# Kernel optimization log

Hardware: AMD Instinct MI355X
Metric: run time of the kernel (lower is better)

The kernel has to match this reference:

```python
import jax, jax.numpy as jnp
import numpy as np
import math

D = 1024
H = 16
HD = D // H
P = 64  # bias_proj_dim
B, N, M = 4, 1024, 2048
EPS_LN = 1e-5
EPS_NORM = 1e-12


def _ln(x, g, b):
    mu = jnp.mean(x, axis=-1, keepdims=True)
    var = jnp.var(x, axis=-1, keepdims=True)
    return (x - mu) * jax.lax.rsqrt(var + EPS_LN) * g + b


def _l2norm_dim1(x):
    # torch F.normalize(x, p=2) default dim=1 -> normalize over the sequence axis
    n = jnp.sqrt(jnp.sum(x * x, axis=1, keepdims=True))
    return x / jnp.maximum(n, EPS_NORM)


def setup_inputs() -> dict:
    key = jax.random.key(0)
    ks = jax.random.split(key, 16)
    s = 1.0 / math.sqrt(D)
    inp = {
        'dataset_features': jax.random.normal(ks[0], (B, N, D), jnp.float32),
        'visual_features': jax.random.normal(ks[1], (B, M, D), jnp.float32),
        # linear weights stored as (in, out): y = x @ W + b
        'wq_w': jax.random.normal(ks[2], (D, D), jnp.float32) * s,
        'wq_b': jnp.zeros((D,), jnp.float32),
        'wk_w': jax.random.normal(ks[3], (D, D), jnp.float32) * s,
        'wk_b': jnp.zeros((D,), jnp.float32),
        'wv_w': jax.random.normal(ks[4], (D, D), jnp.float32) * s,
        'wv_b': jnp.zeros((D,), jnp.float32),
        'wo_w': jax.random.normal(ks[5], (D, D), jnp.float32) * s,
        'wo_b': jnp.zeros((D,), jnp.float32),
        'gq_w': jax.random.normal(ks[6], (D, P), jnp.float32) * s,
        'gq_b': jnp.zeros((P,), jnp.float32),
        'gk_w': jax.random.normal(ks[7], (D, P), jnp.float32) * s,
        'gk_b': jnp.zeros((P,), jnp.float32),
        'pos_scale': jnp.asarray(2.0, jnp.float32),
        'neg_scale': jnp.asarray(50.0, jnp.float32),
        'attn_logit_scale': jnp.asarray(math.log(10.0), jnp.float32),
        'ln_q_g': jnp.ones((D,), jnp.float32),
        'ln_q_b': jnp.zeros((D,), jnp.float32),
        'ln_kv_g': jnp.ones((D,), jnp.float32),
        'ln_kv_b': jnp.zeros((D,), jnp.float32),
        'ln_out_g': jnp.ones((D,), jnp.float32),
        'ln_out_b': jnp.zeros((D,), jnp.float32),
        'ff1_w': jax.random.normal(ks[8], (D, 2 * D), jnp.float32) * s,
        'ff1_b': jnp.zeros((2 * D,), jnp.float32),
        'ff2_w': jax.random.normal(ks[9], (2 * D, D), jnp.float32) * (1.0 / math.sqrt(2 * D)),
        'ff2_b': jnp.zeros((D,), jnp.float32),
    }
    return inp


def reference(dataset_features, visual_features, wq_w, wq_b, wk_w, wk_b, wv_w, wv_b,
              wo_w, wo_b, gq_w, gq_b, gk_w, gk_b, pos_scale, neg_scale,
              attn_logit_scale, ln_q_g, ln_q_b, ln_kv_g, ln_kv_b, ln_out_g, ln_out_b,
              ff1_w, ff1_b, ff2_w, ff2_b):
    residual = dataset_features
    q_in = _ln(dataset_features, ln_q_g, ln_q_b)   # [B,N,D]
    kv_in = _ln(visual_features, ln_kv_g, ln_kv_b)  # [B,M,D]

    geo_q = _l2norm_dim1(q_in @ gq_w + gq_b)   # [B,N,P], normalized over N
    geo_k = _l2norm_dim1(kv_in @ gk_w + gk_b)  # [B,M,P], normalized over M
    bias_raw = jnp.einsum('bnp,bmp->bnm', geo_q, geo_k)  # [B,N,M]
    full_bias = jax.nn.relu(bias_raw) * pos_scale - jax.nn.relu(-bias_raw) * neg_scale

    q = (q_in @ wq_w + wq_b).reshape(B, N, H, HD).transpose(0, 2, 1, 3)   # [B,H,N,hd]
    k = (kv_in @ wk_w + wk_b).reshape(B, M, H, HD).transpose(0, 2, 1, 3)  # [B,H,M,hd]
    v = (kv_in @ wv_w + wv_b).reshape(B, M, H, HD).transpose(0, 2, 1, 3)

    logits = jnp.einsum('bhnd,bhmd->bhnm', q, k) / math.sqrt(HD)
    logits = logits * jnp.exp(attn_logit_scale)
    scores = logits + full_bias[:, None, :, :]
    attn = jax.nn.softmax(scores, axis=-1)
    out = jnp.einsum('bhnm,bhmd->bhnd', attn, v).transpose(0, 2, 1, 3).reshape(B, N, D)
    out = out @ wo_w + wo_b
    out = residual + out

    residual = out
    h = _ln(out, ln_out_g, ln_out_b)
    ff = jax.nn.gelu(h @ ff1_w + ff1_b, approximate=False) @ ff2_w + ff2_b
    return residual + ff
```

## Files before the change

kernel.cpp:

```cpp
#include <hip/hip_runtime.h>


typedef __bf16 bf16x8 __attribute__((ext_vector_type(8)));
typedef __bf16 bf16x4 __attribute__((ext_vector_type(4)));
typedef float  f32x4  __attribute__((ext_vector_type(4)));

__device__ inline f32x4 mfma16(bf16x8 a, bf16x8 b, f32x4 c) {
  return __builtin_amdgcn_mfma_f32_16x16x32_bf16(a, b, c, 0, 0, 0);
}

__device__ inline void glds16(const void* g, void* l) {
  __builtin_amdgcn_global_load_lds(
      (const __attribute__((address_space(1))) void*)g,
      (__attribute__((address_space(3))) void*)l, 16, 0, 0);
}

__device__ inline int swz(int row, int col) {
  return row * 64 + ((((col >> 3) ^ (row & 7)) << 3) | (col & 7));
}

#define DB 1024
#define DH 16
#define DHD 64
#define DP 64
#define NB 4
#define NN 1024
#define NM 2048

__global__ __launch_bounds__(256) void k_transpose_all(
    const float* __restrict__ w0, const float* __restrict__ w1,
    const float* __restrict__ w2, const float* __restrict__ w3,
    const float* __restrict__ f1, const float* __restrict__ f2,
    const float* __restrict__ g0, const float* __restrict__ g1,
    __bf16* __restrict__ o0, __bf16* __restrict__ o1,
    __bf16* __restrict__ o2, __bf16* __restrict__ o3,
    __bf16* __restrict__ of1, __bf16* __restrict__ of2,
    __bf16* __restrict__ og0, __bf16* __restrict__ og1) {
  __shared__ float tile[32][33];
  int id = blockIdx.x;
  const float* in;
  __bf16* out;
  int K, O, x, y;
  if (id < 4096) {
    int mi = id >> 10, r = id & 1023;
    in = mi == 0 ? w0 : mi == 1 ? w1 : mi == 2 ? w2 : w3;
    out = mi == 0 ? o0 : mi == 1 ? o1 : mi == 2 ? o2 : o3;
    K = 1024; O = 1024; x = r & 31; y = r >> 5;
  } else if (id < 6144) {
    int r = id - 4096; in = f1; out = of1; K = 1024; O = 2048; x = r & 63; y = r >> 6;
  } else if (id < 8192) {
    int r = id - 6144; in = f2; out = of2; K = 2048; O = 1024; x = r & 31; y = r >> 5;
  } else if (id < 8256) {
    int r = id - 8192; in = g0; out = og0; K = 1024; O = 64; x = r & 1; y = r >> 1;
  } else {
    int r = id - 8256; in = g1; out = og1; K = 1024; O = 64; x = r & 1; y = r >> 1;
  }
  int k0 = y * 32, o0c = x * 32;
  int tx = threadIdx.x & 31, ty = threadIdx.x >> 5;
#pragma unroll
  for (int r = ty; r < 32; r += 8)
    tile[r][tx] = in[(size_t)(k0 + r) * O + (o0c + tx)];
  __syncthreads();
#pragma unroll
  for (int r = ty; r < 32; r += 8)
    out[(size_t)(o0c + r) * K + (k0 + tx)] = (__bf16)tile[tx][r];
}

__device__ inline void ln_body(const float* __restrict__ x,
                               const float* __restrict__ g,
                               const float* __restrict__ bb,
                               __bf16* __restrict__ y, size_t row) {
  int t = threadIdx.x;
  float4 v = ((const float4*)(x + row * 1024))[t];
  float s = v.x + v.y + v.z + v.w;
  float ss = v.x * v.x + v.y * v.y + v.z * v.z + v.w * v.w;
#pragma unroll
  for (int o = 32; o; o >>= 1) {
    s += __shfl_down(s, o, 64);
    ss += __shfl_down(ss, o, 64);
  }
  __shared__ float r1[4], r2[4];
  if ((t & 63) == 0) { r1[t >> 6] = s; r2[t >> 6] = ss; }
  __syncthreads();
  s = r1[0] + r1[1] + r1[2] + r1[3];
  ss = r2[0] + r2[1] + r2[2] + r2[3];
  float mu = s * (1.f / 1024.f);
  float rstd = rsqrtf(ss * (1.f / 1024.f) - mu * mu + 1e-5f);
  float4 gv = ((const float4*)g)[t];
  float4 bv = ((const float4*)bb)[t];
  __bf16* yr = y + row * 1024 + t * 4;
  yr[0] = (__bf16)((v.x - mu) * rstd * gv.x + bv.x);
  yr[1] = (__bf16)((v.y - mu) * rstd * gv.y + bv.y);
  yr[2] = (__bf16)((v.z - mu) * rstd * gv.z + bv.z);
  yr[3] = (__bf16)((v.w - mu) * rstd * gv.w + bv.w);
}

__global__ __launch_bounds__(256) void k_layernorm(
    const float* __restrict__ x, const float* __restrict__ g,
    const float* __restrict__ bb, __bf16* __restrict__ y) {
  ln_body(x, g, bb, y, blockIdx.x);
}

__global__ __launch_bounds__(256) void k_layernorm2(
    const float* __restrict__ x1, const float* __restrict__ g1,
    const float* __restrict__ b1, __bf16* __restrict__ y1,
    const float* __restrict__ x2, const float* __restrict__ g2,
    const float* __restrict__ b2, __bf16* __restrict__ y2) {
  int row = blockIdx.x;
  if (row < 4096) ln_body(x1, g1, b1, y1, row);
  else ln_body(x2, g2, b2, y2, row - 4096);
}

__global__ __launch_bounds__(256) void k_geo(
    const __bf16* __restrict__ qin, const __bf16* __restrict__ kvin,
    const __bf16* __restrict__ gqw, const __bf16* __restrict__ gkw,
    const float* __restrict__ gqb, const float* __restrict__ gkb,
    __bf16* __restrict__ geoq, __bf16* __restrict__ geok) {
  const int blk = blockIdx.x;
  const bool isq = blk < 128;
  const __bf16* A = isq ? qin : kvin;
  const __bf16* Bt = isq ? gqw : gkw;
  const float* bias = isq ? gqb : gkb;
  __bf16* C = isq ? geoq : geok;
  const int row0 = (isq ? blk : blk - 128) * 32;
  __shared__ __align__(16) __bf16 As[32][72], Bs[64][72];
  const int t = threadIdx.x, lane = t & 63, w = t >> 6;
  const int quad = lane >> 4, l15 = lane & 15;
  const int wr = w >> 1, wc = w & 1;
  const int sr = t >> 3, skc = (t & 7) * 8;
  const __bf16* aP = A + (size_t)(row0 + sr) * 1024 + skc;
  const __bf16* bP0 = Bt + (size_t)sr * 1024 + skc;
  const __bf16* bP1 = Bt + (size_t)(sr + 32) * 1024 + skc;
  bf16x8 av = *(const bf16x8*)aP;
  bf16x8 bv0 = *(const bf16x8*)bP0;
  bf16x8 bv1 = *(const bf16x8*)bP1;
  f32x4 acc[2] = {};
  for (int k0 = 0; k0 < 1024; k0 += 64) {
    __syncthreads();
    *(bf16x8*)&As[sr][skc] = av;
    *(bf16x8*)&Bs[sr][skc] = bv0;
    *(bf16x8*)&Bs[sr + 32][skc] = bv1;
    __syncthreads();
    if (k0 + 64 < 1024) {
      av = *(const bf16x8*)(aP + k0 + 64);
      bv0 = *(const bf16x8*)(bP0 + k0 + 64);
      bv1 = *(const bf16x8*)(bP1 + k0 + 64);
    }
#pragma unroll
    for (int ks = 0; ks < 2; ks++) {
      bf16x8 af = *(const bf16x8*)&As[wr * 16 + l15][ks * 32 + quad * 8];
#pragma unroll
      for (int ct = 0; ct < 2; ct++) {
        bf16x8 bfr = *(const bf16x8*)&Bs[wc * 32 + ct * 16 + l15][ks * 32 + quad * 8];
        acc[ct] = mfma16(af, bfr, acc[ct]);
      }
    }
  }
#pragma unroll
  for (int ct = 0; ct < 2; ct++) {
    int col = wc * 32 + ct * 16 + l15;
    float bc = bias[col];
#pragma unroll
    for (int i = 0; i < 4; i++) {
      int row = row0 + wr * 16 + quad * 4 + i;
      C[(size_t)row * 64 + col] = (__bf16)(acc[ct][i] + bc);
    }
  }
}

__global__ __launch_bounds__(256) void k_l2sum(
    const __bf16* __restrict__ gq, const __bf16* __restrict__ gk,
    float* __restrict__ sums) {
  int chunk = blockIdx.x, b = blockIdx.y, z = blockIdx.z;
  if (z == 0 && chunk >= 8) return;
  const __bf16* src = z ? gk : gq;
  int rows = z ? 2048 : 1024;
  const unsigned* base = (const unsigned*)(src + (size_t)b * rows * 64) + chunk * 128 * 32;
  int t = threadIdx.x, c = t & 31, ro = t >> 5;
  float s0 = 0.f, s1 = 0.f;
  for (int r = ro; r < 128; r += 8) {
    unsigned u = base[r * 32 + c];
    float f0 = __uint_as_float(u << 16);
    float f1 = __uint_as_float(u & 0xffff0000u);
    s0 += f0 * f0;
    s1 += f1 * f1;
  }
  __shared__ float ls[64];
  if (t < 64) ls[t] = 0.f;
  __syncthreads();
  atomicAdd(&ls[c * 2], s0);
  atomicAdd(&ls[c * 2 + 1], s1);
  __syncthreads();
  if (t < 64) atomicAdd(&sums[z * 256 + b * 64 + t], ls[t]);
}

__global__ __launch_bounds__(256) void k_l2scale(
    __bf16* __restrict__ gk, const float* __restrict__ sums) {
  int chunk = blockIdx.x, b = blockIdx.y;
  unsigned* base = (unsigned*)(gk + (size_t)b * 2048 * 64) + chunk * 128 * 32;
  int t = threadIdx.x, c = t & 31, ro = t >> 5;
  float sq0 = sums[b * 64 + c * 2], sq1 = sums[b * 64 + c * 2 + 1];
  float sk0 = sums[256 + b * 64 + c * 2], sk1 = sums[256 + b * 64 + c * 2 + 1];
  float m0 = 1.f / (fmaxf(sqrtf(sq0), 1e-12f) * fmaxf(sqrtf(sk0), 1e-12f));
  float m1 = 1.f / (fmaxf(sqrtf(sq1), 1e-12f) * fmaxf(sqrtf(sk1), 1e-12f));
  for (int r = ro; r < 128; r += 8) {
    unsigned u = base[r * 32 + c];
    float f0 = __uint_as_float(u << 16) * m0;
    float f1 = __uint_as_float(u & 0xffff0000u) * m1;
    unsigned short h0 = __builtin_bit_cast(unsigned short, (__bf16)f0);
    unsigned short h1 = __builtin_bit_cast(unsigned short, (__bf16)f1);
    base[r * 32 + c] = (unsigned)h0 | ((unsigned)h1 << 16);
  }
}

__global__ __launch_bounds__(256) void k_bias(
    const __bf16* __restrict__ gq, const __bf16* __restrict__ gk,
    const float* __restrict__ psc, const float* __restrict__ nsc,
    __bf16* __restrict__ Bias) {
  const int mt0 = blockIdx.x * 128, nt0 = blockIdx.y * 128, b = blockIdx.z;
  const int t = threadIdx.x, lane = t & 63, w = t >> 6;
  const int quad = lane >> 4, l15 = lane & 15;
  const int wm = w & 1, wn = w >> 1;
  const float LOG2E = 1.44269504089f;
  const float pos2 = psc[0] * LOG2E, neg2 = nsc[0] * LOG2E;
  const __bf16* gqb = gq + (size_t)(b * NN + nt0 + wn * 64) * DP;
  const __bf16* gkb = gk + (size_t)(b * NM + mt0 + wm * 64) * DP;
  bf16x8 af[4][2], bg[4][2];
#pragma unroll
  for (int i = 0; i < 4; i++)
#pragma unroll
    for (int ks = 0; ks < 2; ks++) {
      af[i][ks] = *(const bf16x8*)(gkb + (size_t)(i * 16 + l15) * DP + ks * 32 + quad * 8);
      bg[i][ks] = *(const bf16x8*)(gqb + (size_t)(i * 16 + l15) * DP + ks * 32 + quad * 8);
    }
  __bf16* ob = Bias + (size_t)(b * NN + nt0 + wn * 64) * NM + mt0 + wm * 64;
#pragma unroll
  for (int nt = 0; nt < 4; nt++)
#pragma unroll
    for (int mt = 0; mt < 4; mt++) {
      f32x4 acc = {};
      acc = mfma16(af[mt][0], bg[nt][0], acc);
      acc = mfma16(af[mt][1], bg[nt][1], acc);
      bf16x4 o;
#pragma unroll
      for (int i = 0; i < 4; i++) {
        float x = acc[i];
        o[i] = (__bf16)(x > 0.f ? x * pos2 : x * neg2);
      }
      *(bf16x4*)(ob + (size_t)(nt * 16 + l15) * NM + mt * 16 + quad * 4) = o;
    }
}

__global__ __launch_bounds__(256, 3) void k_qkv(
    const __bf16* __restrict__ qin, const __bf16* __restrict__ kvin,
    const __bf16* __restrict__ twq, const __bf16* __restrict__ twk,
    const __bf16* __restrict__ twv, const float* __restrict__ qbias,
    const float* __restrict__ kbias, const float* __restrict__ vbias,
    __bf16* __restrict__ qb, __bf16* __restrict__ kb, __bf16* __restrict__ vtb) {
  int id = blockIdx.x;
  const __bf16 *A, *Bt;
  const float* bias;
  __bf16* C;
  int my, nx, Ndim;
  bool rowbias;
  if (id < 256) {
    A = qin; Bt = twq; bias = qbias; C = qb;
    nx = id & 7; my = id >> 3; Ndim = 1024; rowbias = false;
  } else if (id < 768) {
    id -= 256;
    A = kvin; Bt = twk; bias = kbias; C = kb;
    nx = id & 7; my = id >> 3; Ndim = 1024; rowbias = false;
  } else {
    id -= 768;
    A = twv; Bt = kvin; bias = vbias; C = vtb;
    nx = id & 63; my = id >> 6; Ndim = 8192; rowbias = true;
  }
  const int Kdim = 1024;
  __shared__ __align__(16) __bf16 As[128 * 32];
  __shared__ __align__(16) __bf16 Bs[128 * 32];
  const int m0 = my * 128, n0 = nx * 128;
  const int t = threadIdx.x, lane = t & 63, w = t >> 6;
  const int quad = lane >> 4, l15 = lane & 15;
  const int wr = w >> 1, wc = w & 1;
  const int srow = lane >> 2, scol = (lane & 3) * 8;
  const __bf16* aS0 = A + (size_t)(m0 + w * 32 + srow) * Kdim + scol;
  const __bf16* bS0 = Bt + (size_t)(n0 + w * 32 + srow) * Kdim + scol;
  const size_t K16 = (size_t)16 * Kdim;
  __bf16* lA0 = &As[(w * 32) * 32];
  __bf16* lB0 = &Bs[(w * 32) * 32];

  f32x4 acc[4][4] = {};
  for (int k0 = 0; k0 < Kdim; k0 += 32) {
    __syncthreads();
    glds16(aS0 + k0, lA0);
    glds16(aS0 + K16 + k0, lA0 + 16 * 32);
    glds16(bS0 + k0, lB0);
    glds16(bS0 + K16 + k0, lB0 + 16 * 32);
    __syncthreads();
    bf16x8 af[4], bg[4];
#pragma unroll
    for (int rt = 0; rt < 4; rt++)
      af[rt] = *(const bf16x8*)&As[(wr * 64 + rt * 16 + l15) * 32 + quad * 8];
#pragma unroll
    for (int ct = 0; ct < 4; ct++)
      bg[ct] = *(const bf16x8*)&Bs[(wc * 64 + ct * 16 + l15) * 32 + quad * 8];
#pragma unroll
    for (int rt = 0; rt < 4; rt++)
#pragma unroll
      for (int ct = 0; ct < 4; ct++)
        acc[rt][ct] = mfma16(af[rt], bg[ct], acc[rt][ct]);
  }
#pragma unroll
  for (int rt = 0; rt < 4; rt++) {
    int row = m0 + wr * 64 + rt * 16 + quad * 4;
#pragma unroll
    for (int ct = 0; ct < 4; ct++) {
      int col = n0 + wc * 64 + ct * 16 + l15;
      float bcol = rowbias ? 0.f : bias[col];
#pragma unroll
      for (int i = 0; i < 4; i++) {
        float vv = acc[rt][ct][i] + (rowbias ? bias[row + i] : bcol);
        C[(size_t)(row + i) * Ndim + col] = (__bf16)vv;
      }
    }
  }
}

__global__ __launch_bounds__(256, 3) void k_gemm128g(
    const __bf16* __restrict__ A, const __bf16* __restrict__ Bt,
    const float* __restrict__ bias, __bf16* __restrict__ Cout,
    int Ndim, int Kdim) {
  __shared__ __align__(16) __bf16 As[128 * 32];
  __shared__ __align__(16) __bf16 Bs[128 * 32];
  const int m0 = blockIdx.y * 128, n0 = blockIdx.x * 128;
  const int t = threadIdx.x, lane = t & 63, w = t >> 6;
  const int quad = lane >> 4, l15 = lane & 15;
  const int wr = w >> 1, wc = w & 1;
  const int srow = lane >> 2, scol = (lane & 3) * 8;
  const __bf16* aS0 = A + (size_t)(m0 + w * 32 + srow) * Kdim + scol;
  const __bf16* bS0 = Bt + (size_t)(n0 + w * 32 + srow) * Kdim + scol;
  const size_t K16 = (size_t)16 * Kdim;
  __bf16* lA0 = &As[(w * 32) * 32];
  __bf16* lB0 = &Bs[(w * 32) * 32];

  f32x4 acc[4][4] = {};
  for (int k0 = 0; k0 < Kdim; k0 += 32) {
    __syncthreads();
    glds16(aS0 + k0, lA0);
    glds16(aS0 + K16 + k0, lA0 + 16 * 32);
    glds16(bS0 + k0, lB0);
    glds16(bS0 + K16 + k0, lB0 + 16 * 32);
    __syncthreads();
    bf16x8 af[4], bg[4];
#pragma unroll
    for (int rt = 0; rt < 4; rt++)
      af[rt] = *(const bf16x8*)&As[(wr * 64 + rt * 16 + l15) * 32 + quad * 8];
#pragma unroll
    for (int ct = 0; ct < 4; ct++)
      bg[ct] = *(const bf16x8*)&Bs[(wc * 64 + ct * 16 + l15) * 32 + quad * 8];
#pragma unroll
    for (int rt = 0; rt < 4; rt++)
#pragma unroll
      for (int ct = 0; ct < 4; ct++)
        acc[rt][ct] = mfma16(af[rt], bg[ct], acc[rt][ct]);
  }
#pragma unroll
  for (int rt = 0; rt < 4; rt++) {
    int row = m0 + wr * 64 + rt * 16 + quad * 4;
#pragma unroll
    for (int ct = 0; ct < 4; ct++) {
      int col = n0 + wc * 64 + ct * 16 + l15;
      float bcol = bias[col];
#pragma unroll
      for (int i = 0; i < 4; i++) {
        float vv = acc[rt][ct][i] + bcol;
        Cout[(size_t)(row + i) * Ndim + col] =
            (__bf16)(0.5f * vv * (1.f + erff(vv * 0.70710678118f)));
      }
    }
  }
}

__global__ __launch_bounds__(256, 2) void k_gemmn64(
    const __bf16* __restrict__ A, const __bf16* __restrict__ Bt,
    const float* __restrict__ bias, const float* __restrict__ resid,
    float* __restrict__ Cout, int Ndim, int Kdim) {
  __shared__ __align__(16) __bf16 As[128 * 32];
  __shared__ __align__(16) __bf16 Bs[64 * 32];
  const int m0 = blockIdx.y * 128, n0 = blockIdx.x * 64;
  const int t = threadIdx.x, lane = t & 63, w = t >> 6;
  const int quad = lane >> 4, l15 = lane & 15;
  const int wr = w >> 1, wc = w & 1;
  const int srow = lane >> 2, scol = (lane & 3) * 8;
  const __bf16* aS0 = A + (size_t)(m0 + w * 32 + srow) * Kdim + scol;
  const __bf16* bS0 = Bt + (size_t)(n0 + w * 16 + srow) * Kdim + scol;
  const size_t K16 = (size_t)16 * Kdim;
  __bf16* lA0 = &As[(w * 32) * 32];
  __bf16* lB0 = &Bs[(w * 16) * 32];

  f32x4 acc[4][2] = {};
  for (int k0 = 0; k0 < Kdim; k0 += 32) {
    __syncthreads();
    glds16(aS0 + k0, lA0);
    glds16(aS0 + K16 + k0, lA0 + 16 * 32);
    glds16(bS0 + k0, lB0);
    __syncthreads();
    bf16x8 af[4], bg[2];
#pragma unroll
    for (int rt = 0; rt < 4; rt++)
      af[rt] = *(const bf16x8*)&As[(wr * 64 + rt * 16 + l15) * 32 + quad * 8];
#pragma unroll
    for (int ct = 0; ct < 2; ct++)
      bg[ct] = *(const bf16x8*)&Bs[(wc * 32 + ct * 16 + l15) * 32 + quad * 8];
#pragma unroll
    for (int rt = 0; rt < 4; rt++)
#pragma unroll
      for (int ct = 0; ct < 2; ct++)
        acc[rt][ct] = mfma16(af[rt], bg[ct], acc[rt][ct]);
  }
#pragma unroll
  for (int rt = 0; rt < 4; rt++) {
    int row = m0 + wr * 64 + rt * 16 + quad * 4;
#pragma unroll
    for (int ct = 0; ct < 2; ct++) {
      int col = n0 + wc * 32 + ct * 16 + l15;
      float bcol = bias[col];
#pragma unroll
      for (int i = 0; i < 4; i++) {
        size_t idx = (size_t)(row + i) * Ndim + col;
        Cout[idx] = acc[rt][ct][i] + bcol + resid[idx];
      }
    }
  }
}

__global__ __launch_bounds__(256, 2) void k_flash(
    const __bf16* __restrict__ Q, const __bf16* __restrict__ K,
    const __bf16* __restrict__ Vt, const __bf16* __restrict__ Bias,
    const float* __restrict__ als, __bf16* __restrict__ Out) {
  const int o = blockIdx.x;
  const int bh = o & 63, x = o >> 6;
  const int b = bh & 3, h = bh >> 2;
  const int t = threadIdx.x, w = t >> 6, lane = t & 63;
  const int quad = lane >> 4, l15 = lane & 15;
  const int row0 = x * 128 + w * 32;
  const float LOG2E = 1.44269504089f;
  const float sc2 = __expf(als[0]) * 0.125f * LOG2E;

  __shared__ __align__(16) __bf16 Ks[64 * 64];
  __shared__ __align__(16) __bf16 Vs[64 * 64];
  __shared__ __align__(16) __bf16 Ps[4][32 * 64];

  const __bf16* Qb = Q + ((size_t)(b * NN + row0)) * DB + h * DHD;
  const __bf16* Kb = K + ((size_t)b * NM) * DB + h * DHD;
  const __bf16* Vb = Vt + (size_t)(h * DHD) * (NB * NM) + (size_t)b * NM;
  const __bf16* Bb = Bias + (size_t)(b * NN + row0) * NM;

  const int r0 = t >> 3, gc = (t & 7) * 8;
  const int sw0 = swz(r0, gc), sw1 = sw0 + 32 * 64;
  const int r1 = r0 + 32;

  bf16x8 qf[2][2];
#pragma unroll
  for (int rt = 0; rt < 2; rt++)
#pragma unroll
    for (int ks = 0; ks < 2; ks++)
      qf[rt][ks] = *(const bf16x8*)(Qb + (size_t)(rt * 16 + l15) * DB + ks * 32 + quad * 8);

  bf16x8 kst0 = *(const bf16x8*)(Kb + (size_t)r0 * DB + gc);
  bf16x8 kst1 = *(const bf16x8*)(Kb + (size_t)r1 * DB + gc);
  bf16x8 vst0 = *(const bf16x8*)(Vb + (size_t)r0 * (NB * NM) + gc);
  bf16x8 vst1 = *(const bf16x8*)(Vb + (size_t)r1 * (NB * NM) + gc);

  float lrowq[2] = {};
  f32x4 oacc[2][4] = {};
  f32x4 z4 = {0.f, 0.f, 0.f, 0.f};

  for (int m0 = 0; m0 < NM; m0 += 64) {
    __syncthreads();
    *(bf16x8*)&Ks[sw0] = kst0;
    *(bf16x8*)&Ks[sw1] = kst1;
    *(bf16x8*)&Vs[sw0] = vst0;
    *(bf16x8*)&Vs[sw1] = vst1;
    __syncthreads();
    bf16x4 btv[4][2];
#pragma unroll
    for (int ct = 0; ct < 4; ct++)
#pragma unroll
      for (int rt = 0; rt < 2; rt++)
        btv[ct][rt] = *(const bf16x4*)(Bb + (size_t)(rt * 16 + l15) * NM +
                                       m0 + ct * 16 + quad * 4);
    if (m0 + 64 < NM) {
      kst0 = *(const bf16x8*)(Kb + (size_t)(m0 + 64 + r0) * DB + gc);
      kst1 = *(const bf16x8*)(Kb + (size_t)(m0 + 64 + r1) * DB + gc);
      vst0 = *(const bf16x8*)(Vb + (size_t)r0 * (NB * NM) + m0 + 64 + gc);
      vst1 = *(const bf16x8*)(Vb + (size_t)r1 * (NB * NM) + m0 + 64 + gc);
    }
    bf16x8 kf[4][2];
#pragma unroll
    for (int ct = 0; ct < 4; ct++)
#pragma unroll
      for (int ks = 0; ks < 2; ks++)
        kf[ct][ks] = *(const bf16x8*)&Ks[swz(ct * 16 + l15, ks * 32 + quad * 8)];
#pragma unroll
    for (int ct = 0; ct < 4; ct++)
#pragma unroll
      for (int rt = 0; rt < 2; rt++) {
        f32x4 s = mfma16(kf[ct][1], qf[rt][1], mfma16(kf[ct][0], qf[rt][0], z4));
        bf16x4 pk;
        float part = 0.f;
#pragma unroll
        for (int i = 0; i < 4; i++) {
          float p = __builtin_amdgcn_exp2f(fmaf(s[i], sc2, (float)btv[ct][rt][i]));
          part += p;
          pk[i] = (__bf16)p;
        }
        lrowq[rt] += part;
        *(bf16x4*)&Ps[w][swz(rt * 16 + l15, ct * 16 + quad * 4)] = pk;
      }
    bf16x8 pf[2][2], vf[4][2];
#pragma unroll
    for (int rt = 0; rt < 2; rt++)
#pragma unroll
      for (int ms = 0; ms < 2; ms++)
        pf[rt][ms] = *(const bf16x8*)&Ps[w][swz(rt * 16 + l15, ms * 32 + quad * 8)];
#pragma unroll
    for (int dt = 0; dt < 4; dt++)
#pragma unroll
      for (int ms = 0; ms < 2; ms++)
        vf[dt][ms] = *(const bf16x8*)&Vs[swz(dt * 16 + l15, ms * 32 + quad * 8)];
#pragma unroll
    for (int rt = 0; rt < 2; rt++)
#pragma unroll
      for (int dt = 0; dt < 4; dt++) {
        oacc[rt][dt] = mfma16(pf[rt][0], vf[dt][0], oacc[rt][dt]);
        oacc[rt][dt] = mfma16(pf[rt][1], vf[dt][1], oacc[rt][dt]);
      }
  }
  float ltot[2];
#pragma unroll
  for (int rt = 0; rt < 2; rt++) {
    float l = lrowq[rt];
    l += __shfl_xor(l, 16, 64);
    l += __shfl_xor(l, 32, 64);
    ltot[rt] = l;
  }
#pragma unroll
  for (int rt = 0; rt < 2; rt++)
#pragma unroll
    for (int i = 0; i < 4; i++) {
      float li = __shfl(ltot[rt], quad * 4 + i, 64);
      float inv = 1.f / li;
#pragma unroll
      for (int dt = 0; dt < 4; dt++)
        Out[(size_t)(b * NN + row0 + rt * 16 + quad * 4 + i) * DB + h * DHD + dt * 16 + l15] =
            (__bf16)(oacc[rt][dt][i] * inv);
    }
}

extern "C" void kernel_launch(void* const* d_in, const int* in_sizes, int n_in,
                              void* d_out, int out_size, void* d_ws, size_t ws_size,
                              hipStream_t stream) {
  const float* dataset = (const float*)d_in[0];
  const float* visual = (const float*)d_in[1];
  const float* wq_w = (const float*)d_in[2];
  const float* wq_b = (const float*)d_in[3];
  const float* wk_w = (const float*)d_in[4];
  const float* wk_b = (const float*)d_in[5];
  const float* wv_w = (const float*)d_in[6];
  const float* wv_b = (const float*)d_in[7];
  const float* wo_w = (const float*)d_in[8];
  const float* wo_b = (const float*)d_in[9];
  const float* gq_w = (const float*)d_in[10];
  const float* gq_b = (const float*)d_in[11];
  const float* gk_w = (const float*)d_in[12];
  const float* gk_b = (const float*)d_in[13];
  const float* pos_scale = (const float*)d_in[14];
  const float* neg_scale = (const float*)d_in[15];
  const float* als = (const float*)d_in[16];
  const float* ln_q_g = (const float*)d_in[17];
  const float* ln_q_b = (const float*)d_in[18];
  const float* ln_kv_g = (const float*)d_in[19];
  const float* ln_kv_b = (const float*)d_in[20];
  const float* ln_out_g = (const float*)d_in[21];
  const float* ln_out_b = (const float*)d_in[22];
  const float* ff1_w = (const float*)d_in[23];
  const float* ff1_b = (const float*)d_in[24];
  const float* ff2_w = (const float*)d_in[25];
  const float* ff2_b = (const float*)d_in[26];

  char* ws = (char*)d_ws;
  size_t off = 0;
  auto alloc = [&](size_t bytes) {
    size_t o = off;
    off += (bytes + 255) & ~(size_t)255;
    return o;
  };
  __bf16* t_wq = (__bf16*)(ws + alloc((size_t)1024 * 1024 * 2));
  __bf16* t_wk = (__bf16*)(ws + alloc((size_t)1024 * 1024 * 2));
  __bf16* t_wv = (__bf16*)(ws + alloc((size_t)1024 * 1024 * 2));
  __bf16* t_wo = (__bf16*)(ws + alloc((size_t)1024 * 1024 * 2));
  __bf16* t_ff1 = (__bf16*)(ws + alloc((size_t)2048 * 1024 * 2));
  __bf16* t_ff2 = (__bf16*)(ws + alloc((size_t)1024 * 2048 * 2));
  __bf16* t_gq = (__bf16*)(ws + alloc((size_t)64 * 1024 * 2));
  __bf16* t_gk = (__bf16*)(ws + alloc((size_t)64 * 1024 * 2));
  size_t qin_off = alloc((size_t)4096 * 1024 * 2);
  size_t kvin_off = alloc((size_t)8192 * 1024 * 2);
  __bf16* qin = (__bf16*)(ws + qin_off);
  __bf16* kvin = (__bf16*)(ws + kvin_off);
  __bf16* geoq = (__bf16*)(ws + alloc((size_t)4096 * 64 * 2));
  __bf16* geok = (__bf16*)(ws + alloc((size_t)8192 * 64 * 2));
  float* sums = (float*)(ws + alloc((size_t)2 * 4 * 64 * 4));
  __bf16* biasb = (__bf16*)(ws + alloc((size_t)4096 * 2048 * 2));
  __bf16* qb = (__bf16*)(ws + alloc((size_t)4096 * 1024 * 2));
  __bf16* kb = (__bf16*)(ws + alloc((size_t)8192 * 1024 * 2));
  __bf16* vtb = (__bf16*)(ws + alloc((size_t)1024 * 8192 * 2));
  __bf16* attn = (__bf16*)(ws + alloc((size_t)4096 * 1024 * 2));
  __bf16* ffh = (__bf16*)(ws + alloc((size_t)4096 * 2048 * 2));
  float* out1 = (float*)(ws + kvin_off);
  __bf16* hbuf = (__bf16*)(ws + qin_off);
  float* outp = (float*)d_out;

  dim3 blk(256);
  k_transpose_all<<<8320, blk, 0, stream>>>(wq_w, wk_w, wv_w, wo_w, ff1_w, ff2_w,
                                            gq_w, gk_w, t_wq, t_wk, t_wv, t_wo,
                                            t_ff1, t_ff2, t_gq, t_gk);
  k_layernorm2<<<12288, blk, 0, stream>>>(dataset, ln_q_g, ln_q_b, qin,
                                          visual, ln_kv_g, ln_kv_b, kvin);
  k_geo<<<384, blk, 0, stream>>>(qin, kvin, t_gq, t_gk, gq_b, gk_b, geoq, geok);
  hipMemsetAsync(sums, 0, 2 * 4 * 64 * 4, stream);
  k_l2sum<<<dim3(16, 4, 2), blk, 0, stream>>>(geoq, geok, sums);
  k_l2scale<<<dim3(16, 4), blk, 0, stream>>>(geok, sums);
  k_bias<<<dim3(16, 8, 4), blk, 0, stream>>>(geoq, geok, pos_scale, neg_scale,
                                             biasb);
  k_qkv<<<1280, blk, 0, stream>>>(qin, kvin, t_wq, t_wk, t_wv,
                                  wq_b, wk_b, wv_b, qb, kb, vtb);
  k_flash<<<512, blk, 0, stream>>>(qb, kb, vtb, biasb, als, attn);
  k_gemmn64<<<dim3(16, 32), blk, 0, stream>>>(attn, t_wo, wo_b, dataset, out1,
                                              1024, 1024);
  k_layernorm<<<4096, blk, 0, stream>>>(out1, ln_out_g, ln_out_b, hbuf);
  k_gemm128g<<<dim3(16, 32), blk, 0, stream>>>(hbuf, t_ff1, ff1_b, ffh,
                                               2048, 1024);
  k_gemmn64<<<dim3(16, 32), blk, 0, stream>>>(ffh, t_ff2, ff2_b, out1, outp,
                                              1024, 2048);
}
```

Measured before the change: 451.7 us.

## Split flash attention KV range across wave pairs with register-resident P

Each flash block now handles 64 query rows, with pairs of waves splitting each 64-key tile in halves, and the grid doubles to 1024 blocks. The per-wave P matrix stays in registers and feeds a 16x16x16 MFMA instead of round-tripping through shared memory. K/V tiles are double-buffered in LDS so only one barrier per iteration is needed. Partial outputs and row sums are then combined through shared memory at the end. Launch bounds for k_flash and k_qkv are raised to allow more resident blocks, at the cost of an extra reduction step and tighter register budgets.

```diff
diff --git a/kernel.cpp b/kernel.cpp
--- a/kernel.cpp
+++ b/kernel.cpp
@@ -7,6 +7,13 @@
 
 __device__ inline f32x4 mfma16(bf16x8 a, bf16x8 b, f32x4 c) {
   return __builtin_amdgcn_mfma_f32_16x16x32_bf16(a, b, c, 0, 0, 0);
+}
+
+__device__ inline f32x4 mfma16k16(bf16x4 a, bf16x4 b, f32x4 c) {
+  f32x4 d;
+  asm("v_mfma_f32_16x16x16_bf16 %0, %1, %2, %3"
+      : "=v"(d) : "v"(a), "v"(b), "v"(c));
+  return d;
 }
 
 __device__ inline void glds16(const void* g, void* l) {
@@ -251,7 +258,7 @@
     }
 }
 
-__global__ __launch_bounds__(256, 3) void k_qkv(
+__global__ __launch_bounds__(256, 4) void k_qkv(
     const __bf16* __restrict__ qin, const __bf16* __restrict__ kvin,
     const __bf16* __restrict__ twq, const __bf16* __restrict__ twk,
     const __bf16* __restrict__ twv, const float* __restrict__ qbias,
@@ -434,7 +441,7 @@
   }
 }
 
-__global__ __launch_bounds__(256, 2) void k_flash(
+__global__ __launch_bounds__(256, 4) void k_flash(
     const __bf16* __restrict__ Q, const __bf16* __restrict__ K,
     const __bf16* __restrict__ Vt, const __bf16* __restrict__ Bias,
     const float* __restrict__ als, __bf16* __restrict__ Out) {
@@ -443,18 +450,17 @@
   const int b = bh & 3, h = bh >> 2;
   const int t = threadIdx.x, w = t >> 6, lane = t & 63;
   const int quad = lane >> 4, l15 = lane & 15;
-  const int row0 = x * 128 + w * 32;
-  const float LOG2E = 1.44269504089f;
-  const float sc2 = __expf(als[0]) * 0.125f * LOG2E;
-
-  __shared__ __align__(16) __bf16 Ks[64 * 64];
-  __shared__ __align__(16) __bf16 Vs[64 * 64];
-  __shared__ __align__(16) __bf16 Ps[4][32 * 64];
-
-  const __bf16* Qb = Q + ((size_t)(b * NN + row0)) * DB + h * DHD;
-  const __bf16* Kb = K + ((size_t)b * NM) * DB + h * DHD;
+  const int qh = w >> 1, mh = w & 1;
+  const int row0 = x * 64 + qh * 32;
+  const float sc2 = __expf(als[0]) * 0.125f * 1.44269504089f;
+
+  __shared__ __align__(16) __bf16 smem[16384];
+  __shared__ float Lred[2][64];
+
+  const __bf16* Qb = Q + (size_t)(b * NN + row0) * DB + h * DHD;
+  const __bf16* Kb = K + (size_t)b * NM * DB + h * DHD;
   const __bf16* Vb = Vt + (size_t)(h * DHD) * (NB * NM) + (size_t)b * NM;
-  const __bf16* Bb = Bias + (size_t)(b * NN + row0) * NM;
+  const __bf16* Bb = Bias + (size_t)(b * NN + row0) * NM + mh * 32;
 
   const int r0 = t >> 3, gc = (t & 7) * 8;
   const int sw0 = swz(r0, gc), sw1 = sw0 + 32 * 64;
@@ -467,43 +473,50 @@
     for (int ks = 0; ks < 2; ks++)
       qf[rt][ks] = *(const bf16x8*)(Qb + (size_t)(rt * 16 + l15) * DB + ks * 32 + quad * 8);
 
-  bf16x8 kst0 = *(const bf16x8*)(Kb + (size_t)r0 * DB + gc);
-  bf16x8 kst1 = *(const bf16x8*)(Kb + (size_t)r1 * DB + gc);
-  bf16x8 vst0 = *(const bf16x8*)(Vb + (size_t)r0 * (NB * NM) + gc);
-  bf16x8 vst1 = *(const bf16x8*)(Vb + (size_t)r1 * (NB * NM) + gc);
+  {
+    bf16x8 k0v = *(const bf16x8*)(Kb + (size_t)r0 * DB + gc);
+    bf16x8 k1v = *(const bf16x8*)(Kb + (size_t)r1 * DB + gc);
+    bf16x8 v0v = *(const bf16x8*)(Vb + (size_t)r0 * (NB * NM) + gc);
+    bf16x8 v1v = *(const bf16x8*)(Vb + (size_t)r1 * (NB * NM) + gc);
+    *(bf16x8*)&smem[sw0] = k0v;
+    *(bf16x8*)&smem[sw1] = k1v;
+    *(bf16x8*)&smem[4096 + sw0] = v0v;
+    *(bf16x8*)&smem[4096 + sw1] = v1v;
+  }
 
   float lrowq[2] = {};
   f32x4 oacc[2][4] = {};
   f32x4 z4 = {0.f, 0.f, 0.f, 0.f};
 
-  for (int m0 = 0; m0 < NM; m0 += 64) {
-    __syncthreads();
-    *(bf16x8*)&Ks[sw0] = kst0;
-    *(bf16x8*)&Ks[sw1] = kst1;
-    *(bf16x8*)&Vs[sw0] = vst0;
-    *(bf16x8*)&Vs[sw1] = vst1;
-    __syncthreads();
-    bf16x4 btv[4][2];
-#pragma unroll
-    for (int ct = 0; ct < 4; ct++)
+  for (int it = 0; it < 32; ++it) {
+    const int m0 = it * 64;
+    const int cur = it & 1;
+    __syncthreads();
+    bf16x4 btv[2][2];
+#pragma unroll
+    for (int ct = 0; ct < 2; ct++)
 #pragma unroll
       for (int rt = 0; rt < 2; rt++)
         btv[ct][rt] = *(const bf16x4*)(Bb + (size_t)(rt * 16 + l15) * NM +
                                        m0 + ct * 16 + quad * 4);
-    if (m0 + 64 < NM) {
-      kst0 = *(const bf16x8*)(Kb + (size_t)(m0 + 64 + r0) * DB + gc);
-      kst1 = *(const bf16x8*)(Kb + (size_t)(m0 + 64 + r1) * DB + gc);
-      vst0 = *(const bf16x8*)(Vb + (size_t)r0 * (NB * NM) + m0 + 64 + gc);
-      vst1 = *(const bf16x8*)(Vb + (size_t)r1 * (NB * NM) + m0 + 64 + gc);
-    }
-    bf16x8 kf[4][2];
-#pragma unroll
-    for (int ct = 0; ct < 4; ct++)
+    bf16x8 kn0, kn1, vn0, vn1;
+    if (it + 1 < 32) {
+      kn0 = *(const bf16x8*)(Kb + (size_t)(m0 + 64 + r0) * DB + gc);
+      kn1 = *(const bf16x8*)(Kb + (size_t)(m0 + 64 + r1) * DB + gc);
+      vn0 = *(const bf16x8*)(Vb + (size_t)r0 * (NB * NM) + m0 + 64 + gc);
+      vn1 = *(const bf16x8*)(Vb + (size_t)r1 * (NB * NM) + m0 + 64 + gc);
+    }
+    const __bf16* Kcur = smem + cur * 8192;
+    const __bf16* Vcur = Kcur + 4096;
+    bf16x8 kf[2][2];
+#pragma unroll
+    for (int ct = 0; ct < 2; ct++)
 #pragma unroll
       for (int ks = 0; ks < 2; ks++)
-        kf[ct][ks] = *(const bf16x8*)&Ks[swz(ct * 16 + l15, ks * 32 + quad * 8)];
-#pragma unroll
-    for (int ct = 0; ct < 4; ct++)
+        kf[ct][ks] = *(const bf16x8*)&Kcur[swz(mh * 32 + ct * 16 + l15, ks * 32 + quad * 8)];
+    bf16x4 p[2][2];
+#pragma unroll
+    for (int ct = 0; ct < 2; ct++)
 #pragma unroll
       for (int rt = 0; rt < 2; rt++) {
         f32x4 s = mfma16(kf[ct][1], qf[rt][1], mfma16(kf[ct][0], qf[rt][0], z4));
@@ -511,32 +524,33 @@
         float part = 0.f;
 #pragma unroll
         for (int i = 0; i < 4; i++) {
-          float p = __builtin_amdgcn_exp2f(fmaf(s[i], sc2, (float)btv[ct][rt][i]));
-          part += p;
-          pk[i] = (__bf16)p;
+          float pv = __builtin_amdgcn_exp2f(fmaf(s[i], sc2, (float)btv[ct][rt][i]));
+          part += pv;
+          pk[i] = (__bf16)pv;
         }
         lrowq[rt] += part;
-        *(bf16x4*)&Ps[w][swz(rt * 16 + l15, ct * 16 + quad * 4)] = pk;
-      }
-    bf16x8 pf[2][2], vf[4][2];
-#pragma unroll
-    for (int rt = 0; rt < 2; rt++)
-#pragma unroll
-      for (int ms = 0; ms < 2; ms++)
-        pf[rt][ms] = *(const bf16x8*)&Ps[w][swz(rt * 16 + l15, ms * 32 + quad * 8)];
-#pragma unroll
-    for (int dt = 0; dt < 4; dt++)
-#pragma unroll
-      for (int ms = 0; ms < 2; ms++)
-        vf[dt][ms] = *(const bf16x8*)&Vs[swz(dt * 16 + l15, ms * 32 + quad * 8)];
-#pragma unroll
-    for (int rt = 0; rt < 2; rt++)
+        p[ct][rt] = pk;
+      }
+#pragma unroll
+    for (int ct = 0; ct < 2; ct++)
 #pragma unroll
       for (int dt = 0; dt < 4; dt++) {
-        oacc[rt][dt] = mfma16(pf[rt][0], vf[dt][0], oacc[rt][dt]);
-        oacc[rt][dt] = mfma16(pf[rt][1], vf[dt][1], oacc[rt][dt]);
-      }
-  }
+        bf16x4 vfr = *(const bf16x4*)&Vcur[swz(dt * 16 + l15, mh * 32 + ct * 16 + quad * 4)];
+#pragma unroll
+        for (int rt = 0; rt < 2; rt++)
+          oacc[rt][dt] = mfma16k16(p[ct][rt], vfr, oacc[rt][dt]);
+      }
+    if (it + 1 < 32) {
+      __bf16* dst = smem + (cur ^ 1) * 8192;
+      *(bf16x8*)&dst[sw0] = kn0;
+      *(bf16x8*)&dst[sw1] = kn1;
+      *(bf16x8*)&dst[4096 + sw0] = vn0;
+      *(bf16x8*)&dst[4096 + sw1] = vn1;
+    }
+  }
+
+  __syncthreads();
+  float* Ored = (float*)smem;
   float ltot[2];
 #pragma unroll
   for (int rt = 0; rt < 2; rt++) {
@@ -545,17 +559,36 @@
     l += __shfl_xor(l, 32, 64);
     ltot[rt] = l;
   }
-#pragma unroll
-  for (int rt = 0; rt < 2; rt++)
-#pragma unroll
-    for (int i = 0; i < 4; i++) {
-      float li = __shfl(ltot[rt], quad * 4 + i, 64);
-      float inv = 1.f / li;
+  if (quad == 0) {
+    Lred[mh][qh * 32 + l15] = ltot[0];
+    Lred[mh][qh * 32 + 16 + l15] = ltot[1];
+  }
+  if (mh == 1) {
+#pragma unroll
+    for (int rt = 0; rt < 2; rt++)
 #pragma unroll
       for (int dt = 0; dt < 4; dt++)
-        Out[(size_t)(b * NN + row0 + rt * 16 + quad * 4 + i) * DB + h * DHD + dt * 16 + l15] =
-            (__bf16)(oacc[rt][dt][i] * inv);
-    }
+#pragma unroll
+        for (int i = 0; i < 4; i++)
+          Ored[(qh * 32 + rt * 16 + quad * 4 + i) * 64 + dt * 16 + l15] =
+              oacc[rt][dt][i];
+  }
+  __syncthreads();
+  if (mh == 0) {
+#pragma unroll
+    for (int rt = 0; rt < 2; rt++)
+#pragma unroll
+      for (int i = 0; i < 4; i++) {
+        int r = qh * 32 + rt * 16 + quad * 4 + i;
+        float inv = 1.f / (Lred[0][r] + Lred[1][r]);
+#pragma unroll
+        for (int dt = 0; dt < 4; dt++) {
+          float val = (oacc[rt][dt][i] + Ored[r * 64 + dt * 16 + l15]) * inv;
+          Out[(size_t)(b * NN + x * 64 + r) * DB + h * DHD + dt * 16 + l15] =
+              (__bf16)val;
+        }
+      }
+  }
 }
 
 extern "C" void kernel_launch(void* const* d_in, const int* in_sizes, int n_in,
@@ -635,7 +668,7 @@
                                              biasb);
   k_qkv<<<1280, blk, 0, stream>>>(qin, kvin, t_wq, t_wk, t_wv,
                                   wq_b, wk_b, wv_b, qb, kb, vtb);
-  k_flash<<<512, blk, 0, stream>>>(qb, kb, vtb, biasb, als, attn);
+  k_flash<<<1024, blk, 0, stream>>>(qb, kb, vtb, biasb, als, attn);
   k_gemmn64<<<dim3(16, 32), blk, 0, stream>>>(attn, t_wo, wo_b, dataset, out1,
                                               1024, 1024);
   k_layernorm<<<4096, blk, 0, stream>>>(out1, ln_out_g, ln_out_b, hbuf);
```

Result: slower. 466.4 us (+3.3%).
